# Kernel optimization log

Hardware: AMD Instinct MI355X
Metric: run time of the kernel (lower is better)

Reference implementation:

```python
import jax, jax.numpy as jnp
import numpy as np

H, C, DK = 4, 63, 64   # n_head, context_size, d_k
NF = H * DK            # n_feat = 256


def setup_inputs() -> dict:
    key = jax.random.key(0)
    ks = jax.random.split(key, 7)
    B, T = 2, 4096
    query = jax.random.normal(ks[0], (B, T, NF), jnp.float32)
    key_t = jax.random.normal(ks[1], (B, T, NF), jnp.float32)   # dummy, unused
    value = jax.random.normal(ks[2], (B, T, NF), jnp.float32)
    mask = jnp.ones((B, 1, T), jnp.bool_)                       # dummy, unused
    s = 1.0 / np.sqrt(NF).astype(np.float32)
    w1 = jax.random.normal(ks[3], (NF, NF), jnp.float32) * s
    w2 = jax.random.normal(ks[4], (H * C, NF), jnp.float32) * s
    w3 = jax.random.normal(ks[5], (NF, NF), jnp.float32) * s
    w_out = jax.random.normal(ks[6], (NF, NF), jnp.float32) * s
    return {"query": query, "key": key_t, "value": value, "mask": mask,
            "w1": w1, "w2": w2, "w3": w3, "w_out": w_out}


def reference(query, key, value, mask, w1, w2, w3, w_out):
    # key and mask are dummies (unused), matching the original module.
    B, T, _ = query.shape
    half = (C - 1) // 2

    q = query @ w1.T                                            # (B,T,NF)
    # synthesized band scores: (B,H,T,C)
    weight = (jax.nn.relu(q) @ w2.T).reshape(B, T, H, C).transpose(0, 2, 1, 3)

    # band geometry: score(i, j) lives at offset k = j - i + half, |j-i| <= half
    j_idx = jnp.arange(T)[:, None] + jnp.arange(C)[None, :] - half   # (T,C)
    valid = (j_idx >= 0) & (j_idx < T)                               # (T,C)
    scores = jnp.where(valid[None, None], weight, -jnp.inf)
    p_attn = jax.nn.softmax(scores, axis=-1)                         # (B,H,T,C)

    v = (value @ w3.T).reshape(B, T, H, DK).transpose(0, 2, 1, 3)    # (B,H,T,DK)
    jc = jnp.clip(j_idx, 0, T - 1)                                   # safe gather idx
    windows = v[:, :, jc, :]                                         # (B,H,T,C,DK)
    x = jnp.einsum('bhtc,bhtcd->bhtd', p_attn, windows)              # (B,H,T,DK)

    x = x.transpose(0, 2, 1, 3).reshape(B, T, NF)
    return x @ w_out.T
```

## Files before the change

kernel.cpp:

```cpp
#include <hip/hip_runtime.h>
#include <hip/hip_bf16.h>
#include <math.h>

typedef _Float16 f16x8 __attribute__((ext_vector_type(8)));
typedef _Float16 f16x4 __attribute__((ext_vector_type(4)));
typedef float    f32x4 __attribute__((ext_vector_type(4)));

__device__ __host__ __forceinline__ int swz(int ch, int row) {
    return (ch & 24) | ((ch & 7) ^ (row & 7));
}
__device__ __forceinline__ f32x4 mfma16(f16x8 a, f16x8 b, f32x4 c) {
    return __builtin_amdgcn_mfma_f32_16x16x32_f16(a, b, c, 0, 0, 0);
}
__device__ __forceinline__ f16x8 cvt8(float4 lo, float4 hi) {
    f16x8 r = { (_Float16)lo.x, (_Float16)lo.y, (_Float16)lo.z, (_Float16)lo.w,
                (_Float16)hi.x, (_Float16)hi.y, (_Float16)hi.z, (_Float16)hi.w };
    return r;
}

__global__ __launch_bounds__(256) void convw(const float* __restrict__ w1,
                                             const float* __restrict__ w2,
                                             const float* __restrict__ w3,
                                             const float* __restrict__ wo,
                                             _Float16* __restrict__ p1,
                                             _Float16* __restrict__ p2,
                                             _Float16* __restrict__ p3,
                                             _Float16* __restrict__ po) {
    int gid = blockIdx.x * 256 + threadIdx.x;
    int widx = gid >> 13;
    int r    = gid & 8191;
    int lane = r & 63;
    int ks   = (r >> 6) & 7;
    int nblk = r >> 9;
    int n  = nblk * 16 + (lane & 15);
    int kc = (ks * 4 + (lane >> 4)) * 8;
    const float* src = widx == 0 ? w1 : widx == 1 ? w2 : widx == 2 ? w3 : wo;
    _Float16*    dst = widx == 0 ? p1 : widx == 1 ? p2 : widx == 2 ? p3 : po;
    f16x8 h = {};
    if (!(widx == 1 && n >= 252)) {
        float4 lo = *(const float4*)&src[n * 256 + kc];
        float4 hi = *(const float4*)&src[n * 256 + kc + 4];
        h = cvt8(lo, hi);
    }
    *(f16x8*)&dst[r * 8] = h;
}

__global__ __launch_bounds__(1024, 4) void mono(const float* __restrict__ query,
                                                const float* __restrict__ value,
                                                const _Float16* __restrict__ w1p,
                                                const _Float16* __restrict__ w2p,
                                                const _Float16* __restrict__ w3p,
                                                const _Float16* __restrict__ wop,
                                                float* __restrict__ outp) {
    __shared__ __align__(16) _Float16 RA[16384];
    __shared__ __align__(16) _Float16 RB[8192];
    __shared__ __align__(16) _Float16 Vs[24576];
    __shared__ __align__(16) _Float16 vwT[26624];

    const int tid = threadIdx.x, lane = tid & 63, wid = tid >> 6;
    const int bidr = blockIdx.x;
    const int work = (bidr & 7) * 32 + (bidr >> 3);
    const int b   = work >> 7;
    const int t0  = (work & 127) * 32;
    const size_t rowb = (size_t)b * 4096;

    _Float16* Aq = RA;
    _Float16* Qr = RA + 8192;
    _Float16* Pl = RA;
    _Float16* sc = RB;
    _Float16* xb = RB;

    {
        int row = tid >> 5, ch = tid & 31;
        const float* qp = &query[(rowb + t0 + row) * 256 + ch * 8];
        float4 qlo = *(const float4*)qp, qhi = *(const float4*)(qp + 4);
        float4 vlo[3], vhi[3];
        #pragma unroll
        for (int it = 0; it < 3; ++it) {
            int slot = it * 1024 + tid;
            int vrow = slot >> 5, vch = slot & 31;
            int jl = t0 - 32 + vrow;
            jl = jl < 0 ? 0 : (jl > 4095 ? 4095 : jl);
            const float* p = &value[(rowb + jl) * 256 + vch * 8];
            vlo[it] = *(const float4*)p;
            vhi[it] = *(const float4*)(p + 4);
        }
        *(f16x8*)&Aq[row * 256 + swz(ch, row) * 8] = cvt8(qlo, qhi);
        #pragma unroll
        for (int it = 0; it < 3; ++it) {
            int slot = it * 1024 + tid;
            int vrow = slot >> 5, vch = slot & 31;
            *(f16x8*)&Vs[vrow * 256 + swz(vch, vrow) * 8] = cvt8(vlo[it], vhi[it]);
        }
    }
    __syncthreads();

    {
        f16x8 bfa[8];
        #pragma unroll
        for (int ks = 0; ks < 8; ++ks)
            bfa[ks] = *(const f16x8*)&w1p[((wid * 8 + ks) * 64 + lane) * 8];
        f32x4 acc[2] = {};
        #pragma unroll
        for (int ks = 0; ks < 8; ++ks) {
            int chn = ks * 4 + (lane >> 4);
            #pragma unroll
            for (int i = 0; i < 2; ++i) {
                int row = i * 16 + (lane & 15);
                f16x8 af = *(const f16x8*)&Aq[row * 256 + swz(chn, row) * 8];
                acc[i] = mfma16(af, bfa[ks], acc[i]);
            }
        }
        const int n = wid * 16 + (lane & 15);
        #pragma unroll
        for (int i = 0; i < 2; ++i)
            #pragma unroll
            for (int r = 0; r < 4; ++r) {
                int row = i * 16 + ((lane >> 4) << 2) + r;
                float v = fmaxf(acc[i][r], 0.f);
                Qr[row * 256 + swz(n >> 3, row) * 8 + (n & 7)] = (_Float16)v;
            }
    }
    __syncthreads();

    {
        f16x8 bfa[8];
        #pragma unroll
        for (int ks = 0; ks < 8; ++ks)
            bfa[ks] = *(const f16x8*)&w2p[((wid * 8 + ks) * 64 + lane) * 8];
        f32x4 acc[2] = {};
        #pragma unroll
        for (int ks = 0; ks < 8; ++ks) {
            int chn = ks * 4 + (lane >> 4);
            #pragma unroll
            for (int i = 0; i < 2; ++i) {
                int row = i * 16 + (lane & 15);
                f16x8 af = *(const f16x8*)&Qr[row * 256 + swz(chn, row) * 8];
                acc[i] = mfma16(af, bfa[ks], acc[i]);
            }
        }
        const int n = wid * 16 + (lane & 15);
        #pragma unroll
        for (int i = 0; i < 2; ++i)
            #pragma unroll
            for (int r = 0; r < 4; ++r) {
                int row = i * 16 + ((lane >> 4) << 2) + r;
                sc[row * 256 + swz(n >> 3, row) * 8 + (n & 7)] = (_Float16)acc[i][r];
            }
    }

    {
        f16x8 bfa[8];
        #pragma unroll
        for (int ks = 0; ks < 8; ++ks)
            bfa[ks] = *(const f16x8*)&w3p[((wid * 8 + ks) * 64 + lane) * 8];
        f32x4 a3[6] = {};
        #pragma unroll
        for (int ks = 0; ks < 8; ++ks) {
            int chn = ks * 4 + (lane >> 4);
            #pragma unroll
            for (int mi = 0; mi < 6; ++mi) {
                int row = mi * 16 + (lane & 15);
                f16x8 af = *(const f16x8*)&Vs[row * 256 + swz(chn, row) * 8];
                a3[mi] = mfma16(af, bfa[ks], a3[mi]);
            }
        }
        const int d = wid * 16 + (lane & 15);
        #pragma unroll
        for (int mi = 0; mi < 6; ++mi) {
            int jw = mi * 16 + ((lane >> 4) << 2);
            f16x4 h = { (_Float16)a3[mi][0], (_Float16)a3[mi][1],
                        (_Float16)a3[mi][2], (_Float16)a3[mi][3] };
            *(f16x4*)&vwT[d * 104 + jw] = h;
        }
    }
    __syncthreads();

    const int h = wid >> 2, q = wid & 3;
    #pragma unroll
    for (int it = 0; it < 2; ++it) {
        int s = it * 64 + lane;
        if (s < 104) {
            int rr = h * 32 + q * 8 + s / 13;
            int cc = s % 13;
            f16x8 z = {};
            *(f16x8*)&Pl[rr * 104 + cc * 8] = z;
        }
    }

    {
        const int hf = lane >> 5, c = lane & 31;
        #pragma unroll
        for (int i = 0; i < 4; ++i) {
            int tl = q * 8 + 2 * i + hf;
            int t  = t0 + tl;
            int col0 = h * 63 + c;
            int col1 = col0 + 32;
            int j0 = t + c - 31, j1 = t + c + 1;
            bool ok0 = (j0 >= 0) && (j0 < 4096);
            bool ok1 = (c + 32 < 63) && (j1 >= 0) && (j1 < 4096);
            float s0 = ok0 ? (float)sc[tl * 256 + swz(col0 >> 3, tl) * 8 + (col0 & 7)] : -INFINITY;
            float s1 = ok1 ? (float)sc[tl * 256 + swz(col1 >> 3, tl) * 8 + (col1 & 7)] : -INFINITY;
            float mx = fmaxf(s0, s1);
            #pragma unroll
            for (int off = 16; off > 0; off >>= 1) mx = fmaxf(mx, __shfl_xor(mx, off));
            float e0 = ok0 ? __expf(s0 - mx) : 0.f;
            float e1 = ok1 ? __expf(s1 - mx) : 0.f;
            float sum = e0 + e1;
            #pragma unroll
            for (int off = 16; off > 0; off >>= 1) sum += __shfl_xor(sum, off);
            float inv = 1.0f / sum;
            Pl[(h * 32 + tl) * 104 + (tl + c + 1)] = (_Float16)(e0 * inv);
            if (c + 32 < 63) Pl[(h * 32 + tl) * 104 + (tl + c + 33)] = (_Float16)(e1 * inv);
        }
    }
    __syncthreads();

    {
        const int th = (wid >> 1) & 1, dh = wid & 1;
        f32x4 xa[2] = {};
        #pragma unroll
        for (int ks = 0; ks < 3; ++ks) {
            int chn = ks * 4 + (lane >> 4);
            f16x8 af = *(const f16x8*)&Pl[(h * 32 + th * 16 + (lane & 15)) * 104 + chn * 8];
            #pragma unroll
            for (int j = 0; j < 2; ++j) {
                f16x8 bf = *(const f16x8*)&vwT[(h * 64 + dh * 32 + j * 16 + (lane & 15)) * 104 + chn * 8];
                xa[j] = mfma16(af, bf, xa[j]);
            }
        }
        #pragma unroll
        for (int j = 0; j < 2; ++j)
            #pragma unroll
            for (int r = 0; r < 4; ++r) {
                int row = th * 16 + ((lane >> 4) << 2) + r;
                int n   = h * 64 + dh * 32 + j * 16 + (lane & 15);
                xb[row * 256 + swz(n >> 3, row) * 8 + (n & 7)] = (_Float16)xa[j][r];
            }
    }
    __syncthreads();

    {
        f16x8 bfa[8];
        #pragma unroll
        for (int ks = 0; ks < 8; ++ks)
            bfa[ks] = *(const f16x8*)&wop[((wid * 8 + ks) * 64 + lane) * 8];
        f32x4 oa[2] = {};
        #pragma unroll
        for (int ks = 0; ks < 8; ++ks) {
            int chn = ks * 4 + (lane >> 4);
            #pragma unroll
            for (int i = 0; i < 2; ++i) {
                int row = i * 16 + (lane & 15);
                f16x8 af = *(const f16x8*)&xb[row * 256 + swz(chn, row) * 8];
                oa[i] = mfma16(af, bfa[ks], oa[i]);
            }
        }
        const int n = wid * 16 + (lane & 15);
        #pragma unroll
        for (int i = 0; i < 2; ++i)
            #pragma unroll
            for (int r = 0; r < 4; ++r) {
                int m = t0 + i * 16 + ((lane >> 4) << 2) + r;
                outp[(rowb + m) * 256 + n] = oa[i][r];
            }
    }
}

extern "C" void kernel_launch(void* const* d_in, const int* in_sizes, int n_in,
                              void* d_out, int out_size, void* d_ws, size_t ws_size,
                              hipStream_t stream) {
    const float* query = (const float*)d_in[0];
    const float* value = (const float*)d_in[2];
    const float* w1    = (const float*)d_in[4];
    const float* w2    = (const float*)d_in[5];
    const float* w3    = (const float*)d_in[6];
    const float* w_out = (const float*)d_in[7];

    char* ws = (char*)d_ws;
    _Float16* w1p = (_Float16*)ws;
    _Float16* w2p = w1p + 65536;
    _Float16* w3p = w2p + 65536;
    _Float16* wop = w3p + 65536;

    convw<<<dim3(128), dim3(256), 0, stream>>>(w1, w2, w3, w_out, w1p, w2p, w3p, wop);
    mono<<<dim3(256), dim3(1024), 0, stream>>>(query, value, w1p, w2p, w3p, wop, (float*)d_out);
}
```

Measured before the change: 25.33 us.

## Split value-window load in two halves and overlap the second with early GEMMs

The 96-row value window is now loaded in two 48-row halves instead of all at once. The first half is staged before the first barrier. The second half's global loads are issued before the w1 projection and the w3 projection of the first half, and are written to shared memory only after those GEMMs finish. The aim is to hide global memory latency behind MFMA work, at the cost of more live registers and a split w3 GEMM with duplicated B-fragment loads.

```diff
diff --git a/kernel.cpp b/kernel.cpp
--- a/kernel.cpp
+++ b/kernel.cpp
@@ -74,52 +74,102 @@
         int row = tid >> 5, ch = tid & 31;
         const float* qp = &query[(rowb + t0 + row) * 256 + ch * 8];
         float4 qlo = *(const float4*)qp, qhi = *(const float4*)(qp + 4);
-        float4 vlo[3], vhi[3];
-        #pragma unroll
-        for (int it = 0; it < 3; ++it) {
-            int slot = it * 1024 + tid;
-            int vrow = slot >> 5, vch = slot & 31;
-            int jl = t0 - 32 + vrow;
-            jl = jl < 0 ? 0 : (jl > 4095 ? 4095 : jl);
-            const float* p = &value[(rowb + jl) * 256 + vch * 8];
-            vlo[it] = *(const float4*)p;
-            vhi[it] = *(const float4*)(p + 4);
+        float4 vlo0, vhi0, vlo1, vhi1;
+        int r0 = tid >> 5, c0 = tid & 31;
+        {
+            int jl = t0 - 32 + r0;
+            jl = jl < 0 ? 0 : jl;
+            const float* p = &value[(rowb + jl) * 256 + c0 * 8];
+            vlo0 = *(const float4*)p;  vhi0 = *(const float4*)(p + 4);
+        }
+        int r1 = 0, c1 = 0;
+        if (tid < 512) {
+            int s1 = 1024 + tid;
+            r1 = s1 >> 5;  c1 = s1 & 31;
+            int jl = t0 - 32 + r1;
+            const float* p = &value[(rowb + jl) * 256 + c1 * 8];
+            vlo1 = *(const float4*)p;  vhi1 = *(const float4*)(p + 4);
         }
         *(f16x8*)&Aq[row * 256 + swz(ch, row) * 8] = cvt8(qlo, qhi);
-        #pragma unroll
-        for (int it = 0; it < 3; ++it) {
-            int slot = it * 1024 + tid;
-            int vrow = slot >> 5, vch = slot & 31;
-            *(f16x8*)&Vs[vrow * 256 + swz(vch, vrow) * 8] = cvt8(vlo[it], vhi[it]);
-        }
-    }
-    __syncthreads();
-
-    {
-        f16x8 bfa[8];
-        #pragma unroll
-        for (int ks = 0; ks < 8; ++ks)
-            bfa[ks] = *(const f16x8*)&w1p[((wid * 8 + ks) * 64 + lane) * 8];
-        f32x4 acc[2] = {};
-        #pragma unroll
-        for (int ks = 0; ks < 8; ++ks) {
-            int chn = ks * 4 + (lane >> 4);
-            #pragma unroll
-            for (int i = 0; i < 2; ++i) {
-                int row = i * 16 + (lane & 15);
-                f16x8 af = *(const f16x8*)&Aq[row * 256 + swz(chn, row) * 8];
-                acc[i] = mfma16(af, bfa[ks], acc[i]);
-            }
-        }
-        const int n = wid * 16 + (lane & 15);
-        #pragma unroll
-        for (int i = 0; i < 2; ++i)
-            #pragma unroll
-            for (int r = 0; r < 4; ++r) {
-                int row = i * 16 + ((lane >> 4) << 2) + r;
-                float v = fmaxf(acc[i][r], 0.f);
-                Qr[row * 256 + swz(n >> 3, row) * 8 + (n & 7)] = (_Float16)v;
-            }
+        *(f16x8*)&Vs[r0 * 256 + swz(c0, r0) * 8] = cvt8(vlo0, vhi0);
+        if (tid < 512)
+            *(f16x8*)&Vs[r1 * 256 + swz(c1, r1) * 8] = cvt8(vlo1, vhi1);
+    }
+    __syncthreads();
+
+    {
+        float4 wlo0, whi0, wlo1, whi1;
+        int r0 = 48 + (tid >> 5), c0 = tid & 31;
+        {
+            int jl = t0 - 32 + r0;
+            jl = jl > 4095 ? 4095 : jl;
+            const float* p = &value[(rowb + jl) * 256 + c0 * 8];
+            wlo0 = *(const float4*)p;  whi0 = *(const float4*)(p + 4);
+        }
+        int r1 = 0, c1 = 0;
+        if (tid < 512) {
+            int s1 = 1024 + tid;
+            r1 = 48 + (s1 >> 5);  c1 = s1 & 31;
+            int jl = t0 - 32 + r1;
+            jl = jl > 4095 ? 4095 : jl;
+            const float* p = &value[(rowb + jl) * 256 + c1 * 8];
+            wlo1 = *(const float4*)p;  whi1 = *(const float4*)(p + 4);
+        }
+
+        {
+            f16x8 bfa[8];
+            #pragma unroll
+            for (int ks = 0; ks < 8; ++ks)
+                bfa[ks] = *(const f16x8*)&w1p[((wid * 8 + ks) * 64 + lane) * 8];
+            f32x4 acc[2] = {};
+            #pragma unroll
+            for (int ks = 0; ks < 8; ++ks) {
+                int chn = ks * 4 + (lane >> 4);
+                #pragma unroll
+                for (int i = 0; i < 2; ++i) {
+                    int row = i * 16 + (lane & 15);
+                    f16x8 af = *(const f16x8*)&Aq[row * 256 + swz(chn, row) * 8];
+                    acc[i] = mfma16(af, bfa[ks], acc[i]);
+                }
+            }
+            const int n = wid * 16 + (lane & 15);
+            #pragma unroll
+            for (int i = 0; i < 2; ++i)
+                #pragma unroll
+                for (int r = 0; r < 4; ++r) {
+                    int row = i * 16 + ((lane >> 4) << 2) + r;
+                    float v = fmaxf(acc[i][r], 0.f);
+                    Qr[row * 256 + swz(n >> 3, row) * 8 + (n & 7)] = (_Float16)v;
+                }
+        }
+        {
+            f16x8 bfa[8];
+            #pragma unroll
+            for (int ks = 0; ks < 8; ++ks)
+                bfa[ks] = *(const f16x8*)&w3p[((wid * 8 + ks) * 64 + lane) * 8];
+            f32x4 a3[3] = {};
+            #pragma unroll
+            for (int ks = 0; ks < 8; ++ks) {
+                int chn = ks * 4 + (lane >> 4);
+                #pragma unroll
+                for (int mi = 0; mi < 3; ++mi) {
+                    int row = mi * 16 + (lane & 15);
+                    f16x8 af = *(const f16x8*)&Vs[row * 256 + swz(chn, row) * 8];
+                    a3[mi] = mfma16(af, bfa[ks], a3[mi]);
+                }
+            }
+            const int d = wid * 16 + (lane & 15);
+            #pragma unroll
+            for (int mi = 0; mi < 3; ++mi) {
+                int jw = mi * 16 + ((lane >> 4) << 2);
+                f16x4 h = { (_Float16)a3[mi][0], (_Float16)a3[mi][1],
+                            (_Float16)a3[mi][2], (_Float16)a3[mi][3] };
+                *(f16x4*)&vwT[d * 104 + jw] = h;
+            }
+        }
+        *(f16x8*)&Vs[r0 * 256 + swz(c0, r0) * 8] = cvt8(wlo0, whi0);
+        if (tid < 512)
+            *(f16x8*)&Vs[r1 * 256 + swz(c1, r1) * 8] = cvt8(wlo1, whi1);
     }
     __syncthreads();
 
@@ -148,27 +198,26 @@
                 sc[row * 256 + swz(n >> 3, row) * 8 + (n & 7)] = (_Float16)acc[i][r];
             }
     }
-
     {
         f16x8 bfa[8];
         #pragma unroll
         for (int ks = 0; ks < 8; ++ks)
             bfa[ks] = *(const f16x8*)&w3p[((wid * 8 + ks) * 64 + lane) * 8];
-        f32x4 a3[6] = {};
+        f32x4 a3[3] = {};
         #pragma unroll
         for (int ks = 0; ks < 8; ++ks) {
             int chn = ks * 4 + (lane >> 4);
             #pragma unroll
-            for (int mi = 0; mi < 6; ++mi) {
-                int row = mi * 16 + (lane & 15);
+            for (int mi = 0; mi < 3; ++mi) {
+                int row = 48 + mi * 16 + (lane & 15);
                 f16x8 af = *(const f16x8*)&Vs[row * 256 + swz(chn, row) * 8];
                 a3[mi] = mfma16(af, bfa[ks], a3[mi]);
             }
         }
         const int d = wid * 16 + (lane & 15);
         #pragma unroll
-        for (int mi = 0; mi < 6; ++mi) {
-            int jw = mi * 16 + ((lane >> 4) << 2);
+        for (int mi = 0; mi < 3; ++mi) {
+            int jw = 48 + mi * 16 + ((lane >> 4) << 2);
             f16x4 h = { (_Float16)a3[mi][0], (_Float16)a3[mi][1],
                         (_Float16)a3[mi][2], (_Float16)a3[mi][3] };
             *(f16x4*)&vwT[d * 104 + jw] = h;
```

Result: no change. 25.18 us (-0.6%).
